# Kernel optimization log

Hardware: AMD Instinct MI355X
Metric: run time of the kernel (lower is better)

## Reference

```python
import jax, jax.numpy as jnp
import numpy as np

N_ENVS = 8192
H = W = 64
VIEW = 11
R = VIEW // 2
EMPTY, WALL, FOOD, POISON = 0.0, 1.0, 2.0, 3.0
FOOD_REWARD = 10.0
POISON_PENALTY = 10.0
MOVE_COST = 1.0


def setup_inputs() -> dict:
    key = jax.random.key(0)
    ks = jax.random.split(key, 7)
    grids = jax.random.randint(ks[0], (N_ENVS, H, W), 0, 4).astype(jnp.float32)
    agent_energy = jax.random.uniform(ks[1], (N_ENVS,), minval=1.0, maxval=100.0, dtype=jnp.float32)
    interestingness_lut = jax.random.uniform(ks[2], (5,), dtype=jnp.float32)
    agent_x = jax.random.randint(ks[3], (N_ENVS,), 0, W).astype(jnp.int32)
    agent_y = jax.random.randint(ks[4], (N_ENVS,), 0, H).astype(jnp.int32)
    agent_steps = jax.random.randint(ks[5], (N_ENVS,), 0, 500).astype(jnp.int32)
    actions = jax.random.randint(ks[6], (N_ENVS,), 0, 9).astype(jnp.int32)
    # 3x3 neighborhood moves (dy, dx), matching MAX_MOVE_DISTANCE=1 action space
    action_deltas = jnp.array([[dy, dx] for dy in (-1, 0, 1) for dx in (-1, 0, 1)], dtype=jnp.int32)
    return dict(grids=grids, agent_energy=agent_energy, interestingness_lut=interestingness_lut,
                agent_x=agent_x, agent_y=agent_y, agent_steps=agent_steps,
                actions=actions, action_deltas=action_deltas)


def reference(grids, agent_energy, interestingness_lut, agent_x, agent_y,
              agent_steps, actions, action_deltas):
    n = grids.shape[0]
    env = jnp.arange(n)
    d = action_deltas[actions]                       # (N, 2) = (dy, dx)
    ny = jnp.clip(agent_y + d[:, 0], 0, H - 1)
    nx = jnp.clip(agent_x + d[:, 1], 0, W - 1)
    # block moves into walls: stay in place
    tgt = grids[env, ny, nx]
    blocked = tgt == WALL
    ny = jnp.where(blocked, agent_y, ny)
    nx = jnp.where(blocked, agent_x, nx)
    cell = grids[env, ny, nx]                        # cell agent lands on
    is_food = cell == FOOD
    is_poison = cell == POISON
    reward = jnp.where(is_food, FOOD_REWARD, 0.0) - jnp.where(is_poison, POISON_PENALTY, 0.0)
    consumed = is_food | is_poison
    # scatter: consumed food/poison becomes empty
    new_grids = grids.at[env, ny, nx].set(jnp.where(consumed, EMPTY, cell))
    energy = agent_energy - MOVE_COST + reward
    # local observation windows: pad with WALL, gather (VIEW, VIEW) around agent
    padded = jnp.pad(new_grids, ((0, 0), (R, R), (R, R)), constant_values=WALL)
    win = jax.vmap(lambda g, y, x: jax.lax.dynamic_slice(g, (y, x), (VIEW, VIEW)))(padded, ny, nx)  # (N, V, V)
    f32 = jnp.float32
    obs = jnp.stack([
        (win == FOOD).astype(f32),
        (win == POISON).astype(f32),
        (win == WALL).astype(f32),
        interestingness_lut[win.astype(jnp.int32)],
        win,
        jnp.broadcast_to(energy[:, None, None], (n, VIEW, VIEW)),
    ], axis=1)                                       # (N, 6, V, V)
    return obs
```

## Files before the change

kernel.cpp:

```cpp
#include <hip/hip_runtime.h>

#define NVIEW 11
#define RAD 5
#define GH 64
#define GW 64
#define WINSZ (NVIEW * NVIEW)
#define NCH 6
#define NOUT (NCH * WINSZ)

__global__ __launch_bounds__(256) void env_step_obs_kernel(
    const float* __restrict__ grids,
    const float* __restrict__ agent_energy,
    const float* __restrict__ lut,
    const int*   __restrict__ agent_x,
    const int*   __restrict__ agent_y,
    const int*   __restrict__ actions,
    const int*   __restrict__ action_deltas,
    float*       __restrict__ out,
    int n_envs)
{
    const int lane = threadIdx.x & 63;
    const int wave = threadIdx.x >> 6;
    const int n    = blockIdx.x * 4 + wave;
    if (n >= n_envs) return;

    const int a  = actions[n];
    const int dy = action_deltas[2 * a];
    const int dx = action_deltas[2 * a + 1];
    const int y0 = agent_y[n];
    const int x0 = agent_x[n];

    int ny = min(max(y0 + dy, 0), GH - 1);
    int nx = min(max(x0 + dx, 0), GW - 1);

    const float* g = grids + (size_t)n * (GH * GW);

    const float tgt = g[ny * GW + nx];
    if (tgt == 1.0f) { ny = y0; nx = x0; }

    const float cell      = g[ny * GW + nx];
    const bool  is_food   = (cell == 2.0f);
    const bool  is_poison = (cell == 3.0f);
    const bool  consumed  = is_food || is_poison;
    const float reward    = (is_food ? 10.0f : 0.0f) - (is_poison ? 10.0f : 0.0f);
    const float energy    = agent_energy[n] - 1.0f + reward;

    const float l0 = lut[0], l1 = lut[1], l2 = lut[2], l3 = lut[3];

    float v[2];
    #pragma unroll
    for (int r = 0; r < 2; ++r) {
        const int p = lane + r * 64;
        float val = 1.0f;
        if (p < WINSZ) {
            const int i  = p / NVIEW;
            const int j  = p - i * NVIEW;
            const int yy = ny - RAD + i;
            const int xx = nx - RAD + j;
            if (yy >= 0 && yy < GH && xx >= 0 && xx < GW) val = g[yy * GW + xx];
            if (consumed && p == (RAD * NVIEW + RAD)) val = 0.0f;
        }
        v[r] = val;
    }

    float* ob = out + (size_t)n * NOUT;
    #pragma unroll
    for (int r = 0; r < 2; ++r) {
        const int p = lane + r * 64;
        if (p < WINSZ) {
            const float val = v[r];
            ob[0 * WINSZ + p] = (val == 2.0f) ? 1.0f : 0.0f;
            ob[1 * WINSZ + p] = (val == 3.0f) ? 1.0f : 0.0f;
            ob[2 * WINSZ + p] = (val == 1.0f) ? 1.0f : 0.0f;
            const float lv = (val == 0.0f) ? l0
                           : (val == 1.0f) ? l1
                           : (val == 2.0f) ? l2 : l3;
            ob[3 * WINSZ + p] = lv;
            ob[4 * WINSZ + p] = val;
            ob[5 * WINSZ + p] = energy;
        }
    }
}

extern "C" void kernel_launch(void* const* d_in, const int* in_sizes, int n_in,
                              void* d_out, int out_size, void* d_ws, size_t ws_size,
                              hipStream_t stream) {
    const float* grids   = (const float*)d_in[0];
    const float* energy  = (const float*)d_in[1];
    const float* lut     = (const float*)d_in[2];
    const int*   agent_x = (const int*)d_in[3];
    const int*   agent_y = (const int*)d_in[4];
    const int*   actions = (const int*)d_in[6];
    const int*   deltas  = (const int*)d_in[7];
    float*       out     = (float*)d_out;

    const int n_envs = in_sizes[1];
    const int blocks = (n_envs + 3) / 4;

    env_step_obs_kernel<<<blocks, 256, 0, stream>>>(
        grids, energy, lut, agent_x, agent_y, actions, deltas, out, n_envs);
}
```

Before: 186.1 us.

## Stage observation windows in LDS and emit block output with vectorized nontemporal stores

Each wave now writes its gathered 11x11 window and energy to shared memory. After a barrier, the whole block writes its contiguous output span as float4 nontemporal stores, computing channel and position by integer division. This replaces per-channel scalar stores with some idle lanes by fully packed 16-byte stores. The cost is a block-wide sync, extra index arithmetic, and LDS traffic.

```diff
diff --git a/kernel.cpp b/kernel.cpp
--- a/kernel.cpp
+++ b/kernel.cpp
@@ -7,8 +7,12 @@
 #define WINSZ (NVIEW * NVIEW)
 #define NCH 6
 #define NOUT (NCH * WINSZ)
+#define EPB 4
+#define BLOCK 256
 
-__global__ __launch_bounds__(256) void env_step_obs_kernel(
+typedef __attribute__((ext_vector_type(4))) float f32x4;
+
+__global__ __launch_bounds__(BLOCK) void env_step_obs_kernel(
     const float* __restrict__ grids,
     const float* __restrict__ agent_energy,
     const float* __restrict__ lut,
@@ -19,66 +23,106 @@
     float*       __restrict__ out,
     int n_envs)
 {
-    const int lane = threadIdx.x & 63;
-    const int wave = threadIdx.x >> 6;
-    const int n    = blockIdx.x * 4 + wave;
-    if (n >= n_envs) return;
+    __shared__ float win[EPB][WINSZ + 7];
+    __shared__ float ene[EPB];
 
-    const int a  = actions[n];
-    const int dy = action_deltas[2 * a];
-    const int dx = action_deltas[2 * a + 1];
-    const int y0 = agent_y[n];
-    const int x0 = agent_x[n];
+    const int tid  = threadIdx.x;
+    const int lane = tid & 63;
+    const int wave = tid >> 6;
+    const int n0   = blockIdx.x * EPB;
+    const int n    = n0 + wave;
 
-    int ny = min(max(y0 + dy, 0), GH - 1);
-    int nx = min(max(x0 + dx, 0), GW - 1);
+    if (n < n_envs) {
+        const int a  = actions[n];
+        const int dy = action_deltas[2 * a];
+        const int dx = action_deltas[2 * a + 1];
+        const int y0 = agent_y[n];
+        const int x0 = agent_x[n];
 
-    const float* g = grids + (size_t)n * (GH * GW);
+        int ny = min(max(y0 + dy, 0), GH - 1);
+        int nx = min(max(x0 + dx, 0), GW - 1);
 
-    const float tgt = g[ny * GW + nx];
-    if (tgt == 1.0f) { ny = y0; nx = x0; }
+        const float* g = grids + (size_t)n * (GH * GW);
 
-    const float cell      = g[ny * GW + nx];
-    const bool  is_food   = (cell == 2.0f);
-    const bool  is_poison = (cell == 3.0f);
-    const bool  consumed  = is_food || is_poison;
-    const float reward    = (is_food ? 10.0f : 0.0f) - (is_poison ? 10.0f : 0.0f);
-    const float energy    = agent_energy[n] - 1.0f + reward;
+        const float tgt = g[ny * GW + nx];
+        if (tgt == 1.0f) { ny = y0; nx = x0; }
+
+        const float cell      = g[ny * GW + nx];
+        const bool  is_food   = (cell == 2.0f);
+        const bool  is_poison = (cell == 3.0f);
+        const bool  consumed  = is_food || is_poison;
+        const float reward    = (is_food ? 10.0f : 0.0f) - (is_poison ? 10.0f : 0.0f);
+        if (lane == 0) ene[wave] = agent_energy[n] - 1.0f + reward;
+
+        #pragma unroll
+        for (int r = 0; r < 2; ++r) {
+            const int p = lane + r * 64;
+            if (p < WINSZ) {
+                const int i  = p / NVIEW;
+                const int j  = p - i * NVIEW;
+                const int yy = ny - RAD + i;
+                const int xx = nx - RAD + j;
+                float val = 1.0f;
+                if (yy >= 0 && yy < GH && xx >= 0 && xx < GW) val = g[yy * GW + xx];
+                if (consumed && p == (RAD * NVIEW + RAD)) val = 0.0f;
+                win[wave][p] = val;
+            }
+        }
+    }
+    __syncthreads();
 
     const float l0 = lut[0], l1 = lut[1], l2 = lut[2], l3 = lut[3];
 
-    float v[2];
+    const int valid = min(n_envs - n0, EPB);
+    const int lim   = valid * NOUT;
+    float* base = out + (size_t)n0 * NOUT;
+
     #pragma unroll
-    for (int r = 0; r < 2; ++r) {
-        const int p = lane + r * 64;
-        float val = 1.0f;
-        if (p < WINSZ) {
-            const int i  = p / NVIEW;
-            const int j  = p - i * NVIEW;
-            const int yy = ny - RAD + i;
-            const int xx = nx - RAD + j;
-            if (yy >= 0 && yy < GH && xx >= 0 && xx < GW) val = g[yy * GW + xx];
-            if (consumed && p == (RAD * NVIEW + RAD)) val = 0.0f;
+    for (int round = 0; round < 3; ++round) {
+        const int f = round * (BLOCK * 4) + tid * 4;
+        if (f + 4 <= lim) {
+            f32x4 o;
+            #pragma unroll
+            for (int k = 0; k < 4; ++k) {
+                const int ff  = f + k;
+                const int e   = ff / NOUT;
+                const int rem = ff - e * NOUT;
+                const int c   = rem / WINSZ;
+                const int p   = rem - c * WINSZ;
+                const float val = win[e][p];
+                float ov;
+                if      (c == 0) ov = (val == 2.0f) ? 1.0f : 0.0f;
+                else if (c == 1) ov = (val == 3.0f) ? 1.0f : 0.0f;
+                else if (c == 2) ov = (val == 1.0f) ? 1.0f : 0.0f;
+                else if (c == 3) ov = (val == 0.0f) ? l0
+                                    : (val == 1.0f) ? l1
+                                    : (val == 2.0f) ? l2 : l3;
+                else if (c == 4) ov = val;
+                else             ov = ene[e];
+                o[k] = ov;
+            }
+            __builtin_nontemporal_store(o, reinterpret_cast<f32x4*>(base + f));
         }
-        v[r] = val;
     }
 
-    float* ob = out + (size_t)n * NOUT;
-    #pragma unroll
-    for (int r = 0; r < 2; ++r) {
-        const int p = lane + r * 64;
-        if (p < WINSZ) {
-            const float val = v[r];
-            ob[0 * WINSZ + p] = (val == 2.0f) ? 1.0f : 0.0f;
-            ob[1 * WINSZ + p] = (val == 3.0f) ? 1.0f : 0.0f;
-            ob[2 * WINSZ + p] = (val == 1.0f) ? 1.0f : 0.0f;
-            const float lv = (val == 0.0f) ? l0
-                           : (val == 1.0f) ? l1
-                           : (val == 2.0f) ? l2 : l3;
-            ob[3 * WINSZ + p] = lv;
-            ob[4 * WINSZ + p] = val;
-            ob[5 * WINSZ + p] = energy;
-        }
+    const int tail0 = lim & ~3;
+    if (tid < lim - tail0) {
+        const int ff  = tail0 + tid;
+        const int e   = ff / NOUT;
+        const int rem = ff - e * NOUT;
+        const int c   = rem / WINSZ;
+        const int p   = rem - c * WINSZ;
+        const float val = win[e][p];
+        float ov;
+        if      (c == 0) ov = (val == 2.0f) ? 1.0f : 0.0f;
+        else if (c == 1) ov = (val == 3.0f) ? 1.0f : 0.0f;
+        else if (c == 2) ov = (val == 1.0f) ? 1.0f : 0.0f;
+        else if (c == 3) ov = (val == 0.0f) ? l0
+                            : (val == 1.0f) ? l1
+                            : (val == 2.0f) ? l2 : l3;
+        else if (c == 4) ov = val;
+        else             ov = ene[e];
+        base[ff] = ov;
     }
 }
 
@@ -95,8 +139,8 @@
     float*       out     = (float*)d_out;
 
     const int n_envs = in_sizes[1];
-    const int blocks = (n_envs + 3) / 4;
+    const int blocks = (n_envs + EPB - 1) / EPB;
 
-    env_step_obs_kernel<<<blocks, 256, 0, stream>>>(
+    env_step_obs_kernel<<<blocks, BLOCK, 0, stream>>>(
         grids, energy, lut, agent_x, agent_y, actions, deltas, out, n_envs);
 }
```

Result: no change. 188.5 us (+1.3%).
